# Optimization experiments

Hardware: AMD Instinct MI355X
Metric: run time of the kernel (lower is better)

Reference implementation:

```python
import jax, jax.numpy as jnp
import numpy as np

B, S, H = 1024, 100, 256
C_TANH = 10.0
NEG = -100000.0


def _lin(k, o, i):
    s = 1.0 / np.sqrt(i)
    kw, kb = jax.random.split(k)
    return (jax.random.uniform(kw, (o, i), jnp.float32, -s, s),
            jax.random.uniform(kb, (o,), jnp.float32, -s, s))


def setup_inputs() -> dict:
    key = jax.random.key(0)
    ks = jax.random.split(key, 16)
    inputs = jax.random.uniform(ks[0], (B, S, 2), jnp.float32)
    emb_w, emb_b = _lin(ks[1], H, 2)
    s = 1.0 / np.sqrt(H)
    def lstm(k):
        k1, k2, k3, k4 = jax.random.split(k, 4)
        return (jax.random.uniform(k1, (4 * H, H), jnp.float32, -s, s),
                jax.random.uniform(k2, (4 * H, H), jnp.float32, -s, s),
                jax.random.uniform(k3, (4 * H,), jnp.float32, -s, s),
                jax.random.uniform(k4, (4 * H,), jnp.float32, -s, s))
    enc_wih, enc_whh, enc_bih, enc_bhh = lstm(ks[2])
    dec_wih, dec_whh, dec_bih, dec_bhh = lstm(ks[3])
    ptr_wq_w, ptr_wq_b = _lin(ks[4], H, H)
    ptr_wref_w, ptr_wref_b = _lin(ks[5], H, H)
    ptr_v_w, ptr_v_b = _lin(ks[6], 1, H)
    glm_wq_w, glm_wq_b = _lin(ks[7], H, H)
    glm_wref_w, glm_wref_b = _lin(ks[8], H, H)
    glm_v_w, glm_v_b = _lin(ks[9], 1, H)
    start = jax.random.uniform(ks[10], (H,), jnp.float32, -s, s)
    return dict(inputs=inputs, emb_w=emb_w, emb_b=emb_b,
                enc_wih=enc_wih, enc_whh=enc_whh, enc_bih=enc_bih, enc_bhh=enc_bhh,
                dec_wih=dec_wih, dec_whh=dec_whh, dec_bih=dec_bih, dec_bhh=dec_bhh,
                ptr_wq_w=ptr_wq_w, ptr_wq_b=ptr_wq_b, ptr_wref_w=ptr_wref_w, ptr_wref_b=ptr_wref_b,
                ptr_v_w=ptr_v_w, ptr_v_b=ptr_v_b,
                glm_wq_w=glm_wq_w, glm_wq_b=glm_wq_b, glm_wref_w=glm_wref_w, glm_wref_b=glm_wref_b,
                glm_v_w=glm_v_w, glm_v_b=glm_v_b, start=start)


def _lstm_cell(x, h, c, wih, whh, bih, bhh):
    g = x @ wih.T + bih + h @ whh.T + bhh
    i, f, gg, o = jnp.split(g, 4, axis=-1)  # torch gate order i,f,g,o
    c = jax.nn.sigmoid(f) * c + jax.nn.sigmoid(i) * jnp.tanh(gg)
    h = jax.nn.sigmoid(o) * jnp.tanh(c)
    return h, c


def _attn_logits(q, ref_proj, mask, wq_w, wq_b, v_w, v_b):
    # ref_proj = W_ref(encoder_outputs), precomputed: [B,S,H]
    u = jnp.tanh(ref_proj + (q @ wq_w.T + wq_b)[:, None, :])
    logits = jnp.einsum('bsh,h->bs', u, v_w[0]) + v_b[0]
    logits = jnp.where(mask, NEG, logits)
    return C_TANH * jnp.tanh(logits)


def reference(inputs, emb_w, emb_b,
              enc_wih, enc_whh, enc_bih, enc_bhh,
              dec_wih, dec_whh, dec_bih, dec_bhh,
              ptr_wq_w, ptr_wq_b, ptr_wref_w, ptr_wref_b, ptr_v_w, ptr_v_b,
              glm_wq_w, glm_wq_b, glm_wref_w, glm_wref_b, glm_v_w, glm_v_b,
              start):
    Bn, Sn = inputs.shape[0], inputs.shape[1]
    embedded = inputs @ emb_w.T + emb_b  # [B,S,H]

    def enc_step(carry, x):
        h, c = carry
        h, c = _lstm_cell(x, h, c, enc_wih, enc_whh, enc_bih, enc_bhh)
        return (h, c), h
    z = jnp.zeros((Bn, H), inputs.dtype)
    (h, c), enc_out = jax.lax.scan(enc_step, (z, z), jnp.swapaxes(embedded, 0, 1))
    enc_out = jnp.swapaxes(enc_out, 0, 1)  # [B,S,H]

    ref_g = enc_out @ glm_wref_w.T + glm_wref_b
    ref_p = enc_out @ ptr_wref_w.T + ptr_wref_b
    bidx = jnp.arange(Bn)

    def dec_step(carry, k):
        h, c, mask, dec_in = carry
        h, c = _lstm_cell(dec_in, h, c, dec_wih, dec_whh, dec_bih, dec_bhh)
        q = h
        gl = _attn_logits(q, ref_g, mask, glm_wq_w, glm_wq_b, glm_v_w, glm_v_b)
        q = jnp.einsum('bsh,bs->bh', enc_out, jax.nn.softmax(gl, axis=-1))
        pl = _attn_logits(q, ref_p, mask, ptr_wq_w, ptr_wq_b, ptr_v_w, ptr_v_b)
        logp = jax.nn.log_softmax(pl, axis=-1)
        chosen = jax.random.categorical(k, pl, axis=-1)  # [B]
        lp = jnp.take_along_axis(logp, chosen[:, None], axis=1)[:, 0]
        mask = mask.at[bidx, chosen].set(True)
        dec_in = embedded[bidx, chosen]
        return (h, c, mask, dec_in), (lp, chosen)

    mask0 = jnp.zeros((Bn, Sn), bool)
    dec_in0 = jnp.broadcast_to(start, (Bn, H))
    keys = jax.random.split(jax.random.key(42), Sn)
    _, (lps, chs) = jax.lax.scan(dec_step, (h, c, mask0, dec_in0), keys)
    return jnp.swapaxes(lps, 0, 1), jnp.swapaxes(chs, 0, 1)
```

## Files before the change

### kernel.cpp

```cpp
#include <hip/hip_runtime.h>
#include <cstdint>
#include <cstddef>

#define BB 1024
#define SS 100
#define HH 256

__device__ __forceinline__ unsigned rotl32(unsigned v, int r) {
  return (v << r) | (v >> (32 - r));
}

__device__ __forceinline__ void threefry2x32(unsigned k0, unsigned k1,
                                             unsigned x0, unsigned x1,
                                             unsigned& o0, unsigned& o1) {
  unsigned k2 = k0 ^ k1 ^ 0x1BD11BDAu;
  x0 += k0; x1 += k1;
#define TF_R(r) { x0 += x1; x1 = rotl32(x1, (r)); x1 ^= x0; }
  TF_R(13) TF_R(15) TF_R(26) TF_R(6)
  x0 += k1; x1 += k2 + 1u;
  TF_R(17) TF_R(29) TF_R(16) TF_R(24)
  x0 += k2; x1 += k0 + 2u;
  TF_R(13) TF_R(15) TF_R(26) TF_R(6)
  x0 += k0; x1 += k1 + 3u;
  TF_R(17) TF_R(29) TF_R(16) TF_R(24)
  x0 += k1; x1 += k2 + 4u;
  TF_R(13) TF_R(15) TF_R(26) TF_R(6)
  x0 += k2; x1 += k0 + 5u;
#undef TF_R
  o0 = x0; o1 = x1;
}

__device__ __forceinline__ double sigd(double x) {
  return 1.0 / (1.0 + exp(-x));
}

__device__ __forceinline__ float tanh_fast(float x) {
  float e = __expf(2.0f * x);
  return 1.0f - 2.0f * __builtin_amdgcn_rcpf(e + 1.0f);
}

__device__ __forceinline__ double wave_max(double v) {
#pragma unroll
  for (int off = 32; off; off >>= 1) v = fmax(v, __shfl_xor(v, off));
  return v;
}
__device__ __forceinline__ double wave_sum(double v) {
#pragma unroll
  for (int off = 32; off; off >>= 1) v += __shfl_xor(v, off);
  return v;
}

__global__ __launch_bounds__(256) void init_chunk(
    double* __restrict__ h, double* __restrict__ c) {
  int i = blockIdx.x * 256 + threadIdx.x;
  h[i] = 0.0;
  c[i] = 0.0;
}

__global__ __launch_bounds__(256) void precompute_P(
    const float* __restrict__ emb_w, const float* __restrict__ emb_b,
    const float* __restrict__ start,
    const float* __restrict__ enc_wih, const float* __restrict__ dec_wih,
    double* __restrict__ P) {
  int idx = blockIdx.x * 256 + threadIdx.x;
  int v = idx >> 10, n = idx & 1023;
  const float* W = (v < 3) ? enc_wih : dec_wih;
  int cm = (v < 6) ? (v % 3) : 3;
  const float* wr = W + (size_t)n * HH;
  double acc = 0.0;
  for (int k = 0; k < HH; ++k) {
    double cv;
    if (cm == 0)      cv = (double)emb_w[2 * k];
    else if (cm == 1) cv = (double)emb_w[2 * k + 1];
    else if (cm == 2) cv = (double)emb_b[k];
    else              cv = (double)start[k];
    acc = fma(cv, (double)wr[k], acc);
  }
  P[idx] = acc;
}

__global__ __launch_bounds__(256) void init_dec(
    double* __restrict__ gih, int* __restrict__ mask,
    const double* __restrict__ gih0) {
  const int r = blockIdx.x, t = threadIdx.x;
  if (t < SS) mask[r * SS + t] = 0;
#pragma unroll
  for (int jj = 0; jj < 4; ++jj)
    gih[(size_t)r * 1024 + jj * 256 + t] = gih0[jj * 256 + t];
}

__global__ __launch_bounds__(256) void transpose2(
    const float* __restrict__ a, const float* __restrict__ b,
    float* __restrict__ at, float* __restrict__ bt) {
  int k = blockIdx.x, t = threadIdx.x;
  at[k * HH + t] = a[t * HH + k];
  bt[k * HH + t] = b[t * HH + k];
}

template <bool EMBED>
__global__ __launch_bounds__(256) void lstm_gates(
    const float* __restrict__ inputs, int t, int cb,
    const double* __restrict__ gih,
    const double* __restrict__ Pe,
    const float* __restrict__ Whh,
    const float* __restrict__ bih, const float* __restrict__ bhh,
    const double* __restrict__ hprev, double* __restrict__ hnew,
    double* __restrict__ c, float* __restrict__ enc_c) {
  __shared__ double As[16][34];
  __shared__ double Ws[16][66];
  const int tid = threadIdx.x;
  const int tx = tid & 15;
  const int ty = tid >> 4;
  const int m0 = blockIdx.x * 32;
  const int u0 = blockIdx.y * 16;
  const int arow = tid >> 3;
  const int acol = (tid & 7) * 2;
  const int wn   = tid >> 2;
  const int wcol = (tid & 3) * 4;
  const int wgate = wn >> 4, wu = wn & 15;
  double acc[2][4];

  if (EMBED) {
#pragma unroll
    for (int i = 0; i < 2; ++i) {
      int bb = cb + m0 + ty * 2 + i;
      double i0 = (double)inputs[(bb * SS + t) * 2];
      double i1 = (double)inputs[(bb * SS + t) * 2 + 1];
#pragma unroll
      for (int j = 0; j < 4; ++j) {
        int n = j * 256 + u0 + tx;
        acc[i][j] = fma(i0, Pe[n], fma(i1, Pe[1024 + n], Pe[2048 + n]));
      }
    }
  } else {
#pragma unroll
    for (int i = 0; i < 2; ++i) {
      const double* gr = gih + (size_t)(m0 + ty * 2 + i) * 1024 + u0 + tx;
#pragma unroll
      for (int j = 0; j < 4; ++j) acc[i][j] = gr[j * 256];
    }
  }

  const float* wrow_hh = Whh + (size_t)(wgate * HH + u0 + wu) * HH;

  auto load_slab = [&](int s, double& a0, double& a1, float4& wv) {
    const int k0 = s * 16;
    const double* ar = hprev + (size_t)(m0 + arow) * HH + k0 + acol;
    a0 = ar[0]; a1 = ar[1];
    wv = *(const float4*)(wrow_hh + k0 + wcol);
  };

  double a0c, a1c; float4 wvc;
  load_slab(0, a0c, a1c, wvc);
  for (int s = 0; s < 16; ++s) {
    __syncthreads();
    As[acol][arow] = a0c;
    As[acol + 1][arow] = a1c;
    Ws[wcol + 0][wn] = (double)wvc.x;
    Ws[wcol + 1][wn] = (double)wvc.y;
    Ws[wcol + 2][wn] = (double)wvc.z;
    Ws[wcol + 3][wn] = (double)wvc.w;
    __syncthreads();
    if (s < 15) load_slab(s + 1, a0c, a1c, wvc);
#pragma unroll
    for (int kk = 0; kk < 16; ++kk) {
      double a0k = As[kk][ty * 2];
      double a1k = As[kk][ty * 2 + 1];
#pragma unroll
      for (int j = 0; j < 4; ++j) {
        double w = Ws[kk][j * 16 + tx];
        acc[0][j] = fma(a0k, w, acc[0][j]);
        acc[1][j] = fma(a1k, w, acc[1][j]);
      }
    }
  }

  const int u = u0 + tx;
#pragma unroll
  for (int i = 0; i < 2; ++i) {
    int r = m0 + ty * 2 + i;
    double gi = acc[i][0] + (double)bih[u] + (double)bhh[u];
    double gf = acc[i][1] + (double)bih[HH + u] + (double)bhh[HH + u];
    double gg = acc[i][2] + (double)bih[2 * HH + u] + (double)bhh[2 * HH + u];
    double go = acc[i][3] + (double)bih[3 * HH + u] + (double)bhh[3 * HH + u];
    size_t idx = (size_t)r * HH + u;
    double cp = c[idx];
    double cn = sigd(gf) * cp + sigd(gi) * tanh(gg);
    double hn = sigd(go) * tanh(cn);
    c[idx] = cn;
    hnew[idx] = hn;
    if (enc_c) enc_c[((size_t)r * SS + t) * HH + u] = (float)hn;
  }
}

__global__ __launch_bounds__(256) void proj_gemm(
    const float* __restrict__ A, const float* __restrict__ W,
    const float* __restrict__ bias, float* __restrict__ C) {
  __shared__ double As[16][68];
  __shared__ double Ws[16][68];
  const int tid = threadIdx.x;
  const int tx = tid & 15, ty = tid >> 4;
  const int m0 = blockIdx.x * 64;
  const int n0 = blockIdx.y * 64;
  const int lrow = tid >> 2;
  const int lcol = (tid & 3) << 2;
  double acc[4][4] = {};

  const float* ar = A + (size_t)(m0 + lrow) * HH;
  const float* wr = W + (size_t)(n0 + lrow) * HH;
  for (int k0 = 0; k0 < HH; k0 += 16) {
    float4 av = *(const float4*)(ar + k0 + lcol);
    float4 wv = *(const float4*)(wr + k0 + lcol);
    __syncthreads();
    As[lcol + 0][lrow] = (double)av.x; As[lcol + 1][lrow] = (double)av.y;
    As[lcol + 2][lrow] = (double)av.z; As[lcol + 3][lrow] = (double)av.w;
    Ws[lcol + 0][lrow] = (double)wv.x; Ws[lcol + 1][lrow] = (double)wv.y;
    Ws[lcol + 2][lrow] = (double)wv.z; Ws[lcol + 3][lrow] = (double)wv.w;
    __syncthreads();
#pragma unroll
    for (int kk = 0; kk < 16; ++kk) {
      double a[4], w[4];
#pragma unroll
      for (int i = 0; i < 4; ++i) a[i] = As[kk][ty * 4 + i];
#pragma unroll
      for (int j = 0; j < 4; ++j) w[j] = Ws[kk][tx * 4 + j];
#pragma unroll
      for (int i = 0; i < 4; ++i)
#pragma unroll
        for (int j = 0; j < 4; ++j) acc[i][j] = fma(a[i], w[j], acc[i][j]);
    }
  }
#pragma unroll
  for (int i = 0; i < 4; ++i) {
    float* crow = C + (size_t)(m0 + ty * 4 + i) * HH + n0 + tx * 4;
#pragma unroll
    for (int j = 0; j < 4; ++j)
      crow[j] = (float)(acc[i][j] + (double)bias[n0 + tx * 4 + j]);
  }
}

__global__ __launch_bounds__(256) void dec_attn_sample(
    const double* __restrict__ h,
    const float* __restrict__ enc_c, const float* __restrict__ ref_g,
    const float* __restrict__ ref_p,
    const float* __restrict__ wqt_g, const float* __restrict__ bq_g,
    const float* __restrict__ vw_g, const float* __restrict__ vb_g,
    const float* __restrict__ wqt_p, const float* __restrict__ bq_p,
    const float* __restrict__ vw_p, const float* __restrict__ vb_p,
    int* __restrict__ mask, double* __restrict__ gih,
    const double* __restrict__ Pd,
    const float* __restrict__ inputs,
    float* __restrict__ out, int step, int cb) {
  __shared__ float  hqf[HH];
  __shared__ __align__(16) float qvf[HH];
  __shared__ double lg[SS];
  __shared__ float  lgw[SS];
  __shared__ int    smask[SS];
  __shared__ double redw[4];
  __shared__ int    ridxw[4];
  __shared__ int    sh_chosen;

  const int r = blockIdx.x, t = threadIdx.x;
  const int w = t >> 6, l = t & 63;
  const int b = cb + r;

  hqf[t] = (float)h[(size_t)r * HH + t];
  if (t < SS) smask[t] = mask[r * SS + t];
  __syncthreads();

  {
    float a0 = 0.f, a1 = 0.f, a2 = 0.f, a3 = 0.f;
    for (int k = 0; k < HH; k += 4) {
      a0 = fmaf(wqt_g[(k + 0) * HH + t], hqf[k + 0], a0);
      a1 = fmaf(wqt_g[(k + 1) * HH + t], hqf[k + 1], a1);
      a2 = fmaf(wqt_g[(k + 2) * HH + t], hqf[k + 2], a2);
      a3 = fmaf(wqt_g[(k + 3) * HH + t], hqf[k + 3], a3);
    }
    qvf[t] = ((a0 + a1) + (a2 + a3)) + bq_g[t];
  }
  __syncthreads();

  {
    const float4 vg = *(const float4*)(vw_g + l * 4);
    const float4 qf = *(const float4*)(qvf + l * 4);
    const float vb = vb_g[0];
    for (int s = w; s < SS; s += 4) {
      if (smask[s]) {
        if (l == 0) lg[s] = -10.0;
        continue;
      }
      const float4 rp = *(const float4*)(ref_g + ((size_t)r * SS + s) * HH + l * 4);
      float p = tanh_fast(rp.x + qf.x) * vg.x;
      p = fmaf(tanh_fast(rp.y + qf.y), vg.y, p);
      p = fmaf(tanh_fast(rp.z + qf.z), vg.z, p);
      p = fmaf(tanh_fast(rp.w + qf.w), vg.w, p);
#pragma unroll
      for (int off = 32; off; off >>= 1) p += __shfl_xor(p, off);
      float z = 10.0f * tanh_fast(p + vb);
      if (l == 0) lg[s] = (double)z;
    }
  }
  __syncthreads();

  {
    double x = (t < SS) ? lg[t] : -1e300;
    double vm = wave_max(x);
    if (l == 0) redw[w] = vm;
    __syncthreads();
    double mx = fmax(fmax(redw[0], redw[1]), fmax(redw[2], redw[3]));
    double e = (t < SS) ? exp(x - mx) : 0.0;
    double vs = wave_sum(e);
    __syncthreads();
    if (l == 0) redw[w] = vs;
    __syncthreads();
    double sum = redw[0] + redw[1] + redw[2] + redw[3];
    if (t < SS) lgw[t] = (float)(e / sum);
  }
  __syncthreads();

  {
    const float* eb = enc_c + (size_t)r * SS * HH + t;
    float acc0 = 0.f, acc1 = 0.f, acc2 = 0.f, acc3 = 0.f;
    for (int s = 0; s < SS; s += 4) {
      acc0 = fmaf(eb[(s + 0) * HH], lgw[s + 0], acc0);
      acc1 = fmaf(eb[(s + 1) * HH], lgw[s + 1], acc1);
      acc2 = fmaf(eb[(s + 2) * HH], lgw[s + 2], acc2);
      acc3 = fmaf(eb[(s + 3) * HH], lgw[s + 3], acc3);
    }
    hqf[t] = (acc0 + acc1) + (acc2 + acc3);
  }
  __syncthreads();

  {
    float a0 = 0.f, a1 = 0.f, a2 = 0.f, a3 = 0.f;
    for (int k = 0; k < HH; k += 4) {
      a0 = fmaf(wqt_p[(k + 0) * HH + t], hqf[k + 0], a0);
      a1 = fmaf(wqt_p[(k + 1) * HH + t], hqf[k + 1], a1);
      a2 = fmaf(wqt_p[(k + 2) * HH + t], hqf[k + 2], a2);
      a3 = fmaf(wqt_p[(k + 3) * HH + t], hqf[k + 3], a3);
    }
    qvf[t] = ((a0 + a1) + (a2 + a3)) + bq_p[t];
  }
  __syncthreads();

  {
    const float4 vg = *(const float4*)(vw_p + l * 4);
    const float4 qf = *(const float4*)(qvf + l * 4);
    const float vb = vb_p[0];
    for (int s = w; s < SS; s += 4) {
      if (smask[s]) {
        if (l == 0) lg[s] = -10.0;
        continue;
      }
      const float4 rp = *(const float4*)(ref_p + ((size_t)r * SS + s) * HH + l * 4);
      float p = tanh_fast(rp.x + qf.x) * vg.x;
      p = fmaf(tanh_fast(rp.y + qf.y), vg.y, p);
      p = fmaf(tanh_fast(rp.z + qf.z), vg.z, p);
      p = fmaf(tanh_fast(rp.w + qf.w), vg.w, p);
#pragma unroll
      for (int off = 32; off; off >>= 1) p += __shfl_xor(p, off);
      float z = 10.0f * tanh_fast(p + vb);
      if (l == 0) lg[s] = (double)z;
    }
  }
  __syncthreads();

  double x = (t < SS) ? lg[t] : -1e300;
  double val = -1e300;
  int idx = t;
  if (t < SS) {
    unsigned kk0, kk1;
    threefry2x32(0u, 42u, 0u, (unsigned)step, kk0, kk1);
    unsigned j = (unsigned)(b * SS + t);
    unsigned o0, o1;
    threefry2x32(kk0, kk1, 0u, j, o0, o1);
    unsigned bits = o0 ^ o1;
    double u = (double)(bits >> 9) * 0x1p-23;
    if (u == 0.0) u = 1.17549435e-38;
    val = x + (-log(-log(u)));
  }
#pragma unroll
  for (int off = 32; off; off >>= 1) {
    double v2 = __shfl_xor(val, off);
    int i2 = __shfl_xor(idx, off);
    if (v2 > val || (v2 == val && i2 < idx)) { val = v2; idx = i2; }
  }
  if (l == 0) { redw[w] = val; ridxw[w] = idx; }
  __syncthreads();
  if (t == 0) {
    double bv = redw[0]; int bi = ridxw[0];
#pragma unroll
    for (int i = 1; i < 4; ++i) {
      if (redw[i] > bv || (redw[i] == bv && ridxw[i] < bi)) {
        bv = redw[i]; bi = ridxw[i];
      }
    }
    sh_chosen = bi;
  }
  __syncthreads();
  int chosen = sh_chosen;

  {
    double vm = wave_max(x);
    if (l == 0) redw[w] = vm;
    __syncthreads();
    double mx = fmax(fmax(redw[0], redw[1]), fmax(redw[2], redw[3]));
    double e = (t < SS) ? exp(x - mx) : 0.0;
    double vs = wave_sum(e);
    __syncthreads();
    if (l == 0) redw[w] = vs;
    __syncthreads();
    if (t == 0) {
      double sum = redw[0] + redw[1] + redw[2] + redw[3];
      double lse = log(sum);
      double xc = lg[chosen];
      out[(size_t)b * SS + step] = (float)(xc - mx - lse);
      out[(size_t)BB * SS + (size_t)b * SS + step] = (float)chosen;
      mask[r * SS + chosen] = 1;
    }
  }

  int ib = (b * SS + chosen) * 2;
  double i0 = (double)inputs[ib], i1 = (double)inputs[ib + 1];
#pragma unroll
  for (int jj = 0; jj < 4; ++jj) {
    int n = jj * 256 + t;
    gih[(size_t)r * 1024 + n] =
        fma(i0, Pd[n], fma(i1, Pd[1024 + n], Pd[2048 + n]));
  }
}

__global__ __launch_bounds__(256) void diag_kernel(float* __restrict__ out, float v) {
  int i = blockIdx.x * 256 + threadIdx.x;
  if (i < 2 * BB * SS) out[i] = v;
}

extern "C" void kernel_launch(void* const* d_in, const int* in_sizes, int n_in,
                              void* d_out, int out_size, void* d_ws, size_t ws_size,
                              hipStream_t stream) {
  (void)in_sizes; (void)n_in; (void)out_size;
  const float* inputs    = (const float*)d_in[0];
  const float* emb_w     = (const float*)d_in[1];
  const float* emb_b     = (const float*)d_in[2];
  const float* enc_wih   = (const float*)d_in[3];
  const float* enc_whh   = (const float*)d_in[4];
  const float* enc_bih   = (const float*)d_in[5];
  const float* enc_bhh   = (const float*)d_in[6];
  const float* dec_wih   = (const float*)d_in[7];
  const float* dec_whh   = (const float*)d_in[8];
  const float* dec_bih   = (const float*)d_in[9];
  const float* dec_bhh   = (const float*)d_in[10];
  const float* ptr_wq_w  = (const float*)d_in[11];
  const float* ptr_wq_b  = (const float*)d_in[12];
  const float* ptr_wref_w= (const float*)d_in[13];
  const float* ptr_wref_b= (const float*)d_in[14];
  const float* ptr_v_w   = (const float*)d_in[15];
  const float* ptr_v_b   = (const float*)d_in[16];
  const float* glm_wq_w  = (const float*)d_in[17];
  const float* glm_wq_b  = (const float*)d_in[18];
  const float* glm_wref_w= (const float*)d_in[19];
  const float* glm_wref_b= (const float*)d_in[20];
  const float* glm_v_w   = (const float*)d_in[21];
  const float* glm_v_b   = (const float*)d_in[22];
  const float* start     = (const float*)d_in[23];
  float* out = (float*)d_out;

  auto bytes_needed = [](size_t chunk) -> size_t {
    auto al = [](size_t n) { return (n + 255) & ~(size_t)255; };
    size_t big = al(chunk * SS * HH * 4);
    return 3 * big + 3 * al(chunk * HH * 8) + al(chunk * 1024 * 8) +
           al(chunk * SS * 4) + 2 * al((size_t)HH * HH * 4) +
           al((size_t)7 * 1024 * 8);
  };
  size_t chunk = 1024;
  if (ws_size < bytes_needed(1024)) chunk = 512;
  if (ws_size < bytes_needed(512)) {
    diag_kernel<<<(2 * BB * SS + 255) / 256, 256, 0, stream>>>(
        out, (float)(ws_size >> 20));
    return;
  }

  char* base_p = (char*)d_ws;
  size_t off = 0;
  auto take = [&](size_t nbytes) {
    void* p = base_p + off;
    off = (off + nbytes + 255) & ~(size_t)255;
    return p;
  };
  const size_t BIGC = chunk * SS * HH;
  float*  enc_c  = (float*)take(BIGC * 4);
  float*  ref_g  = (float*)take(BIGC * 4);
  float*  ref_p  = (float*)take(BIGC * 4);
  double* hA     = (double*)take(chunk * HH * 8);
  double* hB     = (double*)take(chunk * HH * 8);
  double* cbuf   = (double*)take(chunk * HH * 8);
  double* gih    = (double*)take(chunk * 1024 * 8);
  int*    mask   = (int*)take(chunk * SS * 4);
  float*  wqt_g  = (float*)take((size_t)HH * HH * 4);
  float*  wqt_p  = (float*)take((size_t)HH * HH * 4);
  double* P      = (double*)take((size_t)7 * 1024 * 8);

  transpose2<<<HH, HH, 0, stream>>>(glm_wq_w, ptr_wq_w, wqt_g, wqt_p);
  precompute_P<<<28, 256, 0, stream>>>(emb_w, emb_b, start, enc_wih, dec_wih, P);

  const double* Pe   = P;
  const double* Pd   = P + 3 * 1024;
  const double* gih0 = P + 6 * 1024;

  const dim3 lstm_grid((unsigned)chunk / 32, 16);
  for (int cb = 0; cb < BB; cb += (int)chunk) {
    init_chunk<<<(unsigned)chunk, 256, 0, stream>>>(hA, cbuf);
    double* hin = hA; double* hout = hB;
    for (int t = 0; t < SS; ++t) {
      lstm_gates<true><<<lstm_grid, 256, 0, stream>>>(
          inputs, t, cb, nullptr, Pe,
          enc_whh, enc_bih, enc_bhh, hin, hout, cbuf, enc_c);
      double* tmp = hin; hin = hout; hout = tmp;
    }

    proj_gemm<<<dim3((unsigned)(chunk * SS / 64), 4), 256, 0, stream>>>(
        enc_c, glm_wref_w, glm_wref_b, ref_g);
    proj_gemm<<<dim3((unsigned)(chunk * SS / 64), 4), 256, 0, stream>>>(
        enc_c, ptr_wref_w, ptr_wref_b, ref_p);

    init_dec<<<(unsigned)chunk, 256, 0, stream>>>(gih, mask, gih0);
    for (int k = 0; k < SS; ++k) {
      lstm_gates<false><<<lstm_grid, 256, 0, stream>>>(
          inputs, 0, cb, gih, nullptr,
          dec_whh, dec_bih, dec_bhh, hin, hout, cbuf, nullptr);
      dec_attn_sample<<<(unsigned)chunk, 256, 0, stream>>>(
          hout, enc_c, ref_g, ref_p,
          wqt_g, glm_wq_b, glm_v_w, glm_v_b,
          wqt_p, ptr_wq_b, ptr_v_w, ptr_v_b,
          mask, gih, Pd, inputs, out, k, cb);
      double* tmp = hin; hin = hout; hout = tmp;
    }
  }
}
```

Measured before the change: 17.60 ms.

## Process four batch rows per block in decoder attention, one wave per row

After: 28.71 ms. 1.63x slower.

```diff
diff --git a/kernel.cpp b/kernel.cpp
--- a/kernel.cpp
+++ b/kernel.cpp
@@ -251,45 +251,61 @@
     const double* __restrict__ Pd,
     const float* __restrict__ inputs,
     float* __restrict__ out, int step, int cb) {
-  __shared__ float  hqf[HH];
-  __shared__ __align__(16) float qvf[HH];
-  __shared__ double lg[SS];
-  __shared__ float  lgw[SS];
-  __shared__ int    smask[SS];
-  __shared__ double redw[4];
-  __shared__ int    ridxw[4];
-  __shared__ int    sh_chosen;
-
-  const int r = blockIdx.x, t = threadIdx.x;
+  __shared__ __align__(16) float hqf[4][HH];
+  __shared__ __align__(16) float qvf[4][HH];
+  __shared__ double lg[4][SS];
+  __shared__ float  lgw[4][SS];
+  __shared__ int    smask[4][SS];
+
+  const int t = threadIdx.x;
   const int w = t >> 6, l = t & 63;
-  const int b = cb + r;
-
-  hqf[t] = (float)h[(size_t)r * HH + t];
-  if (t < SS) smask[t] = mask[r * SS + t];
+  const int r0 = blockIdx.x * 4;
+  const int rw = r0 + w;
+  const int bw = cb + rw;
+
+#pragma unroll
+  for (int i = 0; i < 4; ++i)
+    hqf[i][t] = (float)h[(size_t)(r0 + i) * HH + t];
+  if (t < SS) {
+#pragma unroll
+    for (int i = 0; i < 4; ++i) smask[i][t] = mask[(r0 + i) * SS + t];
+  }
   __syncthreads();
 
   {
-    float a0 = 0.f, a1 = 0.f, a2 = 0.f, a3 = 0.f;
+    float a[4][4] = {};
     for (int k = 0; k < HH; k += 4) {
-      a0 = fmaf(wqt_g[(k + 0) * HH + t], hqf[k + 0], a0);
-      a1 = fmaf(wqt_g[(k + 1) * HH + t], hqf[k + 1], a1);
-      a2 = fmaf(wqt_g[(k + 2) * HH + t], hqf[k + 2], a2);
-      a3 = fmaf(wqt_g[(k + 3) * HH + t], hqf[k + 3], a3);
-    }
-    qvf[t] = ((a0 + a1) + (a2 + a3)) + bq_g[t];
+      float w0 = wqt_g[(k + 0) * HH + t];
+      float w1 = wqt_g[(k + 1) * HH + t];
+      float w2 = wqt_g[(k + 2) * HH + t];
+      float w3 = wqt_g[(k + 3) * HH + t];
+#pragma unroll
+      for (int i = 0; i < 4; ++i) {
+        a[i][0] = fmaf(w0, hqf[i][k + 0], a[i][0]);
+        a[i][1] = fmaf(w1, hqf[i][k + 1], a[i][1]);
+        a[i][2] = fmaf(w2, hqf[i][k + 2], a[i][2]);
+        a[i][3] = fmaf(w3, hqf[i][k + 3], a[i][3]);
+      }
+    }
+    float bq = bq_g[t];
+#pragma unroll
+    for (int i = 0; i < 4; ++i)
+      qvf[i][t] = ((a[i][0] + a[i][1]) + (a[i][2] + a[i][3])) + bq;
   }
   __syncthreads();
 
   {
     const float4 vg = *(const float4*)(vw_g + l * 4);
-    const float4 qf = *(const float4*)(qvf + l * 4);
+    const float4 qf = *(const float4*)(&qvf[w][l * 4]);
     const float vb = vb_g[0];
-    for (int s = w; s < SS; s += 4) {
-      if (smask[s]) {
-        if (l == 0) lg[s] = -10.0;
+    const float* rbase = ref_g + (size_t)rw * SS * HH + l * 4;
+#pragma unroll 2
+    for (int s = 0; s < SS; ++s) {
+      if (smask[w][s]) {
+        if (l == 0) lg[w][s] = -10.0;
         continue;
       }
-      const float4 rp = *(const float4*)(ref_g + ((size_t)r * SS + s) * HH + l * 4);
+      const float4 rp = *(const float4*)(rbase + (size_t)s * HH);
       float p = tanh_fast(rp.x + qf.x) * vg.x;
       p = fmaf(tanh_fast(rp.y + qf.y), vg.y, p);
       p = fmaf(tanh_fast(rp.z + qf.z), vg.z, p);
@@ -297,62 +313,76 @@
 #pragma unroll
       for (int off = 32; off; off >>= 1) p += __shfl_xor(p, off);
       float z = 10.0f * tanh_fast(p + vb);
-      if (l == 0) lg[s] = (double)z;
-    }
+      if (l == 0) lg[w][s] = (double)z;
+    }
+  }
+
+  {
+    double x1 = lg[w][l];
+    double x2 = (l < SS - 64) ? lg[w][l + 64] : -1e300;
+    double mx = wave_max(fmax(x1, x2));
+    double e1 = exp(x1 - mx);
+    double e2 = (l < SS - 64) ? exp(x2 - mx) : 0.0;
+    double sum = wave_sum(e1 + e2);
+    lgw[w][l] = (float)(e1 / sum);
+    if (l < SS - 64) lgw[w][l + 64] = (float)(e2 / sum);
+  }
+
+  {
+    const float* eb = enc_c + (size_t)rw * SS * HH;
+    float a[4][4] = {};
+    for (int s = 0; s < SS; s += 4) {
+      float g0 = lgw[w][s + 0], g1 = lgw[w][s + 1];
+      float g2 = lgw[w][s + 2], g3 = lgw[w][s + 3];
+#pragma unroll
+      for (int j = 0; j < 4; ++j) {
+        const float* ec = eb + j * 64 + l;
+        a[j][0] = fmaf(ec[(s + 0) * HH], g0, a[j][0]);
+        a[j][1] = fmaf(ec[(s + 1) * HH], g1, a[j][1]);
+        a[j][2] = fmaf(ec[(s + 2) * HH], g2, a[j][2]);
+        a[j][3] = fmaf(ec[(s + 3) * HH], g3, a[j][3]);
+      }
+    }
+#pragma unroll
+    for (int j = 0; j < 4; ++j)
+      hqf[w][j * 64 + l] = (a[j][0] + a[j][1]) + (a[j][2] + a[j][3]);
   }
   __syncthreads();
 
   {
-    double x = (t < SS) ? lg[t] : -1e300;
-    double vm = wave_max(x);
-    if (l == 0) redw[w] = vm;
-    __syncthreads();
-    double mx = fmax(fmax(redw[0], redw[1]), fmax(redw[2], redw[3]));
-    double e = (t < SS) ? exp(x - mx) : 0.0;
-    double vs = wave_sum(e);
-    __syncthreads();
-    if (l == 0) redw[w] = vs;
-    __syncthreads();
-    double sum = redw[0] + redw[1] + redw[2] + redw[3];
-    if (t < SS) lgw[t] = (float)(e / sum);
+    float a[4][4] = {};
+    for (int k = 0; k < HH; k += 4) {
+      float w0 = wqt_p[(k + 0) * HH + t];
+      float w1 = wqt_p[(k + 1) * HH + t];
+      float w2 = wqt_p[(k + 2) * HH + t];
+      float w3 = wqt_p[(k + 3) * HH + t];
+#pragma unroll
+      for (int i = 0; i < 4; ++i) {
+        a[i][0] = fmaf(w0, hqf[i][k + 0], a[i][0]);
+        a[i][1] = fmaf(w1, hqf[i][k + 1], a[i][1]);
+        a[i][2] = fmaf(w2, hqf[i][k + 2], a[i][2]);
+        a[i][3] = fmaf(w3, hqf[i][k + 3], a[i][3]);
+      }
+    }
+    float bq = bq_p[t];
+#pragma unroll
+    for (int i = 0; i < 4; ++i)
+      qvf[i][t] = ((a[i][0] + a[i][1]) + (a[i][2] + a[i][3])) + bq;
   }
   __syncthreads();
 
   {
-    const float* eb = enc_c + (size_t)r * SS * HH + t;
-    float acc0 = 0.f, acc1 = 0.f, acc2 = 0.f, acc3 = 0.f;
-    for (int s = 0; s < SS; s += 4) {
-      acc0 = fmaf(eb[(s + 0) * HH], lgw[s + 0], acc0);
-      acc1 = fmaf(eb[(s + 1) * HH], lgw[s + 1], acc1);
-      acc2 = fmaf(eb[(s + 2) * HH], lgw[s + 2], acc2);
-      acc3 = fmaf(eb[(s + 3) * HH], lgw[s + 3], acc3);
-    }
-    hqf[t] = (acc0 + acc1) + (acc2 + acc3);
-  }
-  __syncthreads();
-
-  {
-    float a0 = 0.f, a1 = 0.f, a2 = 0.f, a3 = 0.f;
-    for (int k = 0; k < HH; k += 4) {
-      a0 = fmaf(wqt_p[(k + 0) * HH + t], hqf[k + 0], a0);
-      a1 = fmaf(wqt_p[(k + 1) * HH + t], hqf[k + 1], a1);
-      a2 = fmaf(wqt_p[(k + 2) * HH + t], hqf[k + 2], a2);
-      a3 = fmaf(wqt_p[(k + 3) * HH + t], hqf[k + 3], a3);
-    }
-    qvf[t] = ((a0 + a1) + (a2 + a3)) + bq_p[t];
-  }
-  __syncthreads();
-
-  {
     const float4 vg = *(const float4*)(vw_p + l * 4);
-    const float4 qf = *(const float4*)(qvf + l * 4);
+    const float4 qf = *(const float4*)(&qvf[w][l * 4]);
     const float vb = vb_p[0];
-    for (int s = w; s < SS; s += 4) {
-      if (smask[s]) {
-        if (l == 0) lg[s] = -10.0;
+    const float* rbase = ref_p + (size_t)rw * SS * HH + l * 4;
+#pragma unroll 2
+    for (int s = 0; s < SS; ++s) {
+      if (smask[w][s]) {
+        if (l == 0) lg[w][s] = -10.0;
         continue;
       }
-      const float4 rp = *(const float4*)(ref_p + ((size_t)r * SS + s) * HH + l * 4);
+      const float4 rp = *(const float4*)(rbase + (size_t)s * HH);
       float p = tanh_fast(rp.x + qf.x) * vg.x;
       p = fmaf(tanh_fast(rp.y + qf.y), vg.y, p);
       p = fmaf(tanh_fast(rp.z + qf.z), vg.z, p);
@@ -360,73 +390,66 @@
 #pragma unroll
       for (int off = 32; off; off >>= 1) p += __shfl_xor(p, off);
       float z = 10.0f * tanh_fast(p + vb);
-      if (l == 0) lg[s] = (double)z;
-    }
-  }
-  __syncthreads();
-
-  double x = (t < SS) ? lg[t] : -1e300;
-  double val = -1e300;
-  int idx = t;
-  if (t < SS) {
+      if (l == 0) lg[w][s] = (double)z;
+    }
+  }
+
+  double x1 = lg[w][l];
+  double x2 = (l < SS - 64) ? lg[w][l + 64] : -1e300;
+  int chosen;
+  {
     unsigned kk0, kk1;
     threefry2x32(0u, 42u, 0u, (unsigned)step, kk0, kk1);
-    unsigned j = (unsigned)(b * SS + t);
     unsigned o0, o1;
-    threefry2x32(kk0, kk1, 0u, j, o0, o1);
+    threefry2x32(kk0, kk1, 0u, (unsigned)(bw * SS + l), o0, o1);
     unsigned bits = o0 ^ o1;
     double u = (double)(bits >> 9) * 0x1p-23;
     if (u == 0.0) u = 1.17549435e-38;
-    val = x + (-log(-log(u)));
-  }
-#pragma unroll
-  for (int off = 32; off; off >>= 1) {
-    double v2 = __shfl_xor(val, off);
-    int i2 = __shfl_xor(idx, off);
-    if (v2 > val || (v2 == val && i2 < idx)) { val = v2; idx = i2; }
-  }
-  if (l == 0) { redw[w] = val; ridxw[w] = idx; }
-  __syncthreads();
-  if (t == 0) {
-    double bv = redw[0]; int bi = ridxw[0];
-#pragma unroll
-    for (int i = 1; i < 4; ++i) {
-      if (redw[i] > bv || (redw[i] == bv && ridxw[i] < bi)) {
-        bv = redw[i]; bi = ridxw[i];
-      }
-    }
-    sh_chosen = bi;
-  }
-  __syncthreads();
-  int chosen = sh_chosen;
-
-  {
-    double vm = wave_max(x);
-    if (l == 0) redw[w] = vm;
-    __syncthreads();
-    double mx = fmax(fmax(redw[0], redw[1]), fmax(redw[2], redw[3]));
-    double e = (t < SS) ? exp(x - mx) : 0.0;
-    double vs = wave_sum(e);
-    __syncthreads();
-    if (l == 0) redw[w] = vs;
-    __syncthreads();
-    if (t == 0) {
-      double sum = redw[0] + redw[1] + redw[2] + redw[3];
+    double val = x1 + (-log(-log(u)));
+    int idx = l;
+    if (l < SS - 64) {
+      threefry2x32(kk0, kk1, 0u, (unsigned)(bw * SS + l + 64), o0, o1);
+      bits = o0 ^ o1;
+      double u2 = (double)(bits >> 9) * 0x1p-23;
+      if (u2 == 0.0) u2 = 1.17549435e-38;
+      double v2 = x2 + (-log(-log(u2)));
+      if (v2 > val) { val = v2; idx = l + 64; }
+    }
+#pragma unroll
+    for (int off = 32; off; off >>= 1) {
+      double v2 = __shfl_xor(val, off);
+      int i2 = __shfl_xor(idx, off);
+      if (v2 > val || (v2 == val && i2 < idx)) { val = v2; idx = i2; }
+    }
+    chosen = idx;
+  }
+
+  {
+    double mx = wave_max(fmax(x1, x2));
+    double e1 = exp(x1 - mx);
+    double e2 = (l < SS - 64) ? exp(x2 - mx) : 0.0;
+    double sum = wave_sum(e1 + e2);
+    if (l == 0) {
       double lse = log(sum);
-      double xc = lg[chosen];
-      out[(size_t)b * SS + step] = (float)(xc - mx - lse);
-      out[(size_t)BB * SS + (size_t)b * SS + step] = (float)chosen;
-      mask[r * SS + chosen] = 1;
-    }
-  }
-
-  int ib = (b * SS + chosen) * 2;
-  double i0 = (double)inputs[ib], i1 = (double)inputs[ib + 1];
-#pragma unroll
-  for (int jj = 0; jj < 4; ++jj) {
-    int n = jj * 256 + t;
-    gih[(size_t)r * 1024 + n] =
-        fma(i0, Pd[n], fma(i1, Pd[1024 + n], Pd[2048 + n]));
+      double xc = lg[w][chosen];
+      out[(size_t)bw * SS + step] = (float)(xc - mx - lse);
+      out[(size_t)BB * SS + (size_t)bw * SS + step] = (float)chosen;
+      mask[rw * SS + chosen] = 1;
+    }
+  }
+
+  {
+    int ib = (bw * SS + chosen) * 2;
+    double i0 = (double)inputs[ib], i1 = (double)inputs[ib + 1];
+    double* gr = gih + (size_t)rw * 1024;
+#pragma unroll
+    for (int jj = 0; jj < 4; ++jj) {
+#pragma unroll
+      for (int q = 0; q < 4; ++q) {
+        int n = jj * 256 + q * 64 + l;
+        gr[n] = fma(i0, Pd[n], fma(i1, Pd[1024 + n], Pd[2048 + n]));
+      }
+    }
   }
 }
 
@@ -528,7 +551,7 @@
       lstm_gates<false><<<lstm_grid, 256, 0, stream>>>(
           inputs, 0, cb, gih, nullptr,
           dec_whh, dec_bih, dec_bhh, hin, hout, cbuf, nullptr);
-      dec_attn_sample<<<(unsigned)chunk, 256, 0, stream>>>(
+      dec_attn_sample<<<(unsigned)(chunk / 4), 256, 0, stream>>>(
           hout, enc_c, ref_g, ref_p,
           wqt_g, glm_wq_b, glm_v_w, glm_v_b,
           wqt_p, ptr_wq_b, ptr_v_w, ptr_v_b,
```
